# Optimization experiments

Measured on AMD Instinct MI355X. Metric: run time of the kernel, lower is better.

Reference implementation:

```python
import jax, jax.numpy as jnp
import numpy as np

# NOTE: PersistentHomology / wasserstein_distance are not in the provided source.
# We implement the standard interpretation: H0 (0-dimensional) persistent homology
# of the Vietoris-Rips filtration on the pairwise Euclidean distance matrix, whose
# diagram is (birth=0, death=w) for each edge weight w of the minimum spanning tree
# (single-linkage). The 1-Wasserstein distance between two equal-cardinality
# diagrams with birth=0 reduces to the L1 distance between sorted death values.

MARGIN = 1.0
EPS = 1e-12


def _pairwise_dist(x):
    # x: [N, D] -> [N, N] Euclidean distances
    sq = jnp.sum(x * x, axis=-1)
    d2 = sq[:, None] + sq[None, :] - 2.0 * (x @ x.T)
    return jnp.sqrt(jnp.maximum(d2, EPS))


def _mst_deaths(dist):
    # Prim's algorithm on the dense distance matrix; returns the N-1 MST edge
    # weights = H0 death times of the Vietoris-Rips filtration.
    n = dist.shape[0]
    inf = jnp.asarray(1e30, dist.dtype)
    visited0 = jnp.zeros(n, dtype=bool).at[0].set(True)
    mind0 = dist[0]  # min distance from current tree to every vertex

    def step(carry, _):
        visited, mind = carry
        cand = jnp.where(visited, inf, mind)
        j = jnp.argmin(cand)          # next vertex to attach
        w = cand[j]                   # weight of the MST edge used
        visited = visited.at[j].set(True)
        mind = jnp.minimum(mind, dist[j])
        return (visited, mind), w

    _, deaths = jax.lax.scan(step, (visited0, mind0), None, length=n - 1)
    return deaths  # [N-1]


def _wasserstein_1d(d1, d2):
    # 1-Wasserstein between two equal-size H0 diagrams (births are all 0):
    # optimal matching of 1-D point sets = L1 between sorted values.
    return jnp.sum(jnp.abs(jnp.sort(d1) - jnp.sort(d2)))


def _topological_distance(x, y):
    return _wasserstein_1d(_mst_deaths(_pairwise_dist(x)), _mst_deaths(_pairwise_dist(y)))


def setup_inputs() -> dict:
    key = jax.random.key(0)
    ka, kp, kn = jax.random.split(key, 3)
    N, D = 4096, 1024
    return {
        "anchor": jax.random.normal(ka, (N, D), dtype=jnp.float32),
        "positive": jax.random.normal(kp, (N, D), dtype=jnp.float32),
        "negative": jax.random.normal(kn, (N, D), dtype=jnp.float32),
    }


def reference(anchor, positive, negative):
    pos_dist = _topological_distance(anchor, positive)
    neg_dist = _topological_distance(anchor, negative)
    return jnp.maximum(pos_dist - neg_dist + MARGIN, 0.0)
```

## Files before the change

kernel.cpp:

```cpp
#include <hip/hip_runtime.h>
#include <stdint.h>


#define NPTS 4096
#define DIMF 1024
typedef unsigned short u16;
typedef _Float16 f16;
typedef unsigned long long ull;
static const ull KEY_MAX_ULL = ~0ull;

typedef f16 f16x8 __attribute__((ext_vector_type(8)));
typedef f16 f16x4v __attribute__((ext_vector_type(4)));
typedef float f32x4 __attribute__((ext_vector_type(4)));

#define GLOAD_LDS16(g, l)                                                      \
  __builtin_amdgcn_global_load_lds(                                            \
      (const __attribute__((address_space(1))) void*)(g),                      \
      (__attribute__((address_space(3))) void*)(l), 16, 0, 0)

__global__ void k_init_global(int* __restrict__ comp, ull* __restrict__ best,
                              float* __restrict__ deaths, int* __restrict__ cnt) {
  const int i = blockIdx.x * blockDim.x + threadIdx.x;
  if (i < 3 * NPTS) {
    comp[i] = i & (NPTS - 1);
    best[i] = KEY_MAX_ULL;
    deaths[i] = __int_as_float(0x7f800000);
  }
  if (i < 16) cnt[i] = 0;
}

__global__ __launch_bounds__(256)
void k_prep(const float* __restrict__ x, float* __restrict__ sq,
            f16* __restrict__ hi) {
  const int row = blockIdx.x;
  const int t = threadIdx.x;
  const float4 v = ((const float4*)(x + (size_t)row * DIMF))[t];
  f16x4v h;
  h.x = (f16)v.x; h.y = (f16)v.y; h.z = (f16)v.z; h.w = (f16)v.w;
  ((f16x4v*)(hi + (size_t)row * DIMF))[t] = h;
  float s = v.x * v.x + v.y * v.y + v.z * v.z + v.w * v.w;
  for (int off = 32; off > 0; off >>= 1) s += __shfl_xor(s, off, 64);
  __shared__ float ws[4];
  if ((t & 63) == 0) ws[t >> 6] = s;
  __syncthreads();
  if (t == 0) sq[row] = ws[0] + ws[1] + ws[2] + ws[3];
}

__global__ __launch_bounds__(256)
void k_gemm_f16(const f16* __restrict__ hi, const float* __restrict__ sq,
                f16* __restrict__ d16) {
  __shared__ u16 smem[8192];
  u16* As = smem;
  u16* Bs = smem + 4096;
  const int t = threadIdx.x;
  const int w = t >> 6, l = t & 63;
  const int wm = w >> 1, wn = w & 1;
  const int ml = l & 15, kq = l >> 4;
  const int i0 = blockIdx.y * 128, j0 = blockIdx.x * 128;

  const int srow = t >> 2, schk = t & 3;
  char* ldsA0 = (char*)As + t * 16;
  char* ldsB0 = (char*)Bs + t * 16;

  f32x4 acc[4][4];
#pragma unroll
  for (int a = 0; a < 4; ++a)
#pragma unroll
    for (int b = 0; b < 4; ++b) acc[a][b] = (f32x4)0.f;

  for (int k0 = 0; k0 < DIMF; k0 += 32) {
    __syncthreads();
    {
      const f16* ga0 = hi + (size_t)(i0 + srow) * DIMF + k0 + schk * 8;
      const f16* ga1 = hi + (size_t)(i0 + srow + 64) * DIMF + k0 + schk * 8;
      const f16* gb0 = hi + (size_t)(j0 + srow) * DIMF + k0 + schk * 8;
      const f16* gb1 = hi + (size_t)(j0 + srow + 64) * DIMF + k0 + schk * 8;
      GLOAD_LDS16(ga0, ldsA0);
      GLOAD_LDS16(ga1, ldsA0 + 4096);
      GLOAD_LDS16(gb0, ldsB0);
      GLOAD_LDS16(gb1, ldsB0 + 4096);
    }
    asm volatile("s_waitcnt vmcnt(0)" ::: "memory");
    __syncthreads();

    const char* Ab = (const char*)As + (wm * 64 + ml) * 64 + kq * 16;
    const char* Bb = (const char*)Bs + (wn * 64 + ml) * 64 + kq * 16;
    f16x8 af[4], bf[4];
#pragma unroll
    for (int mt = 0; mt < 4; ++mt) af[mt] = *(const f16x8*)(Ab + mt * 1024);
#pragma unroll
    for (int nt = 0; nt < 4; ++nt) bf[nt] = *(const f16x8*)(Bb + nt * 1024);
#pragma unroll
    for (int mt = 0; mt < 4; ++mt)
#pragma unroll
      for (int nt = 0; nt < 4; ++nt)
        acc[mt][nt] = __builtin_amdgcn_mfma_f32_16x16x32_f16(
            af[mt], bf[nt], acc[mt][nt], 0, 0, 0);
  }

  float sr[4][4], sc[4];
#pragma unroll
  for (int mt = 0; mt < 4; ++mt)
#pragma unroll
    for (int r = 0; r < 4; ++r)
      sr[mt][r] = sq[i0 + wm * 64 + mt * 16 + kq * 4 + r];
#pragma unroll
  for (int nt = 0; nt < 4; ++nt) sc[nt] = sq[j0 + wn * 64 + nt * 16 + ml];

#pragma unroll
  for (int mt = 0; mt < 4; ++mt)
#pragma unroll
    for (int nt = 0; nt < 4; ++nt) {
      const int col = j0 + wn * 64 + nt * 16 + ml;
#pragma unroll
      for (int r = 0; r < 4; ++r) {
        const int row = i0 + wm * 64 + mt * 16 + kq * 4 + r;
        const float v = fmaxf(sr[mt][r] + sc[nt] - 2.f * acc[mt][nt][r], 0.f);
        d16[(size_t)row * NPTS + col] = (f16)v;
      }
    }
}

__global__ __launch_bounds__(256)
void k_scan3(const u16* __restrict__ d16, const int* __restrict__ comp,
             ull* __restrict__ best, const int* __restrict__ done) {
  const int b = blockIdx.x;
  const int c = b >> 12;
  const int i = b & (NPTS - 1);
  if (done[c]) return;
  const int t = threadIdx.x;
  __shared__ ull red[4];
  const int* compc = comp + c * NPTS;
  int cj[16];
  {
    const int4* cp = (const int4*)compc;
    const int4 a0 = cp[t * 4 + 0], a1 = cp[t * 4 + 1];
    const int4 a2 = cp[t * 4 + 2], a3 = cp[t * 4 + 3];
    cj[0] = a0.x;  cj[1] = a0.y;  cj[2] = a0.z;  cj[3] = a0.w;
    cj[4] = a1.x;  cj[5] = a1.y;  cj[6] = a1.z;  cj[7] = a1.w;
    cj[8] = a2.x;  cj[9] = a2.y;  cj[10] = a2.z; cj[11] = a2.w;
    cj[12] = a3.x; cj[13] = a3.y; cj[14] = a3.z; cj[15] = a3.w;
  }
  const int ci = compc[i];
  const uint4* rp =
      (const uint4*)(d16 + (size_t)c * NPTS * NPTS + (size_t)i * NPTS);
  const uint4 Aw = rp[t * 2 + 0], Bw = rp[t * 2 + 1];
  const unsigned wds[8] = {Aw.x, Aw.y, Aw.z, Aw.w, Bw.x, Bw.y, Bw.z, Bw.w};
  ull kmin = KEY_MAX_ULL;
#pragma unroll
  for (int u = 0; u < 8; ++u) {
    const int j0c = t * 16 + u * 2;
    const unsigned lo = wds[u] & 0xFFFFu;
    const unsigned hi2 = wds[u] >> 16;
    if (cj[u * 2] != ci) {
      const int j = j0c;
      const ull pair = (i < j) ? (((ull)i << 12) | (unsigned)j)
                               : (((ull)j << 12) | (unsigned)i);
      const ull key = ((ull)lo << 24) | pair;
      kmin = (key < kmin) ? key : kmin;
    }
    if (cj[u * 2 + 1] != ci) {
      const int j = j0c + 1;
      const ull pair = (i < j) ? (((ull)i << 12) | (unsigned)j)
                               : (((ull)j << 12) | (unsigned)i);
      const ull key = ((ull)hi2 << 24) | pair;
      kmin = (key < kmin) ? key : kmin;
    }
  }
  for (int off = 32; off > 0; off >>= 1) {
    const ull o = __shfl_xor(kmin, off, 64);
    kmin = (o < kmin) ? o : kmin;
  }
  if ((t & 63) == 0) red[t >> 6] = kmin;
  __syncthreads();
  if (t == 0) {
    ull k2 = red[0];
    k2 = (red[1] < k2) ? red[1] : k2;
    k2 = (red[2] < k2) ? red[2] : k2;
    k2 = (red[3] < k2) ? red[3] : k2;
    if (k2 != KEY_MAX_ULL) atomicMin(best + c * NPTS + ci, k2);
  }
}

__global__ __launch_bounds__(1024)
void k_merge3(ull* __restrict__ best, int* __restrict__ comp,
              int* __restrict__ comp2, int* __restrict__ pairs,
              int* __restrict__ cnt, int* __restrict__ done,
              int* __restrict__ Cdev, ull* __restrict__ cd, int initCd) {
  const int c = blockIdx.x;
  if (done[c]) return;
  ull* bestc = best + c * NPTS;
  int* compc = comp + c * NPTS;
  int* comp2c = comp2 + c * NPTS;
  int* pairsc = pairs + c * NPTS;
  __shared__ int par[NPTS];
  __shared__ int hk[NPTS];
  __shared__ int redi[16];
  __shared__ int chg;
  __shared__ int cdense;
  const int t = threadIdx.x;
  ull bb[4];
#pragma unroll
  for (int s = 0; s < 4; ++s) {
    const int v = t + s * 1024;
    par[v] = compc[v];
    bb[s] = bestc[v];
    bestc[v] = KEY_MAX_ULL;
  }
  __syncthreads();
#pragma unroll
  for (int s = 0; s < 4; ++s) {
    const int v = t + s * 1024;
    const ull b2 = bb[s];
    int h;
    if (b2 == KEY_MAX_ULL) {
      h = par[v];
    } else {
      const int pair = (int)(b2 & 0xFFFFFF);
      const int a = pair >> 12, c2 = pair & 4095;
      const int ra = par[a], rb = par[c2];
      h = (ra == v) ? rb : ra;
    }
    hk[v] = h;
  }
  __syncthreads();
  bool win[4];
#pragma unroll
  for (int s = 0; s < 4; ++s) {
    const int v = t + s * 1024;
    const ull b2 = bb[s];
    win[s] = false;
    if (b2 != KEY_MAX_ULL) {
      const int so = hk[v];
      const bool mut = (hk[so] == v);
      win[s] = mut && (v < so);
      if (!mut || v < so)
        pairsc[atomicAdd(cnt + c, 1)] = (int)(b2 & 0xFFFFFF);
    }
  }
  if (t == 0) chg = 0;
  __syncthreads();
#pragma unroll
  for (int s = 0; s < 4; ++s)
    if (win[s]) hk[t + s * 1024] = t + s * 1024;
  __syncthreads();
  for (int it = 0; it < 12; ++it) {
    int w2[4]; int ch = 0;
#pragma unroll
    for (int s = 0; s < 4; ++s) {
      const int v = t + s * 1024;
      w2[s] = hk[hk[v]];
      ch |= (w2[s] != hk[v]);
    }
    __syncthreads();
#pragma unroll
    for (int s = 0; s < 4; ++s) hk[t + s * 1024] = w2[s];
    if (ch) chg = 1;
    __syncthreads();
    const int any = chg;
    __syncthreads();
    if (t == 0) chg = 0;
    if (!any) break;
  }
  int nroot = 0;
#pragma unroll
  for (int s = 0; s < 4; ++s) {
    const int v = t + s * 1024;
    const int rv = hk[v];
    compc[v] = rv;
    nroot += (rv == v);
  }
  for (int off = 32; off > 0; off >>= 1) nroot += __shfl_xor(nroot, off, 64);
  if ((t & 63) == 0) redi[t >> 6] = nroot;
  if (t == 0) cdense = 0;
  __syncthreads();
#pragma unroll
  for (int s = 0; s < 4; ++s) {
    const int v = t + s * 1024;
    if (hk[v] == v) par[v] = atomicAdd(&cdense, 1);
  }
  __syncthreads();
#pragma unroll
  for (int s = 0; s < 4; ++s) {
    const int v = t + s * 1024;
    comp2c[v] = par[hk[v]];
  }
  if (initCd) {
    ull* cdc = cd + (size_t)c * 65536;
    for (int q = t; q < 65536; q += 1024) cdc[q] = KEY_MAX_ULL;
  }
  if (t == 0) {
    int tot = 0;
    for (int q = 0; q < 16; ++q) tot += redi[q];
    Cdev[c] = cdense;
    if (tot == 1) done[c] = 1;
  }
}

__global__ __launch_bounds__(256)
void k_contract3(const u16* __restrict__ d16, const int* __restrict__ comp2,
                 ull* __restrict__ cd, const int* __restrict__ done) {
  const int b = blockIdx.x;
  const int c = b >> 12;
  const int i = b & (NPTS - 1);
  if (done[c]) return;
  const int t = threadIdx.x;
  __shared__ ull tbl[256];
  tbl[t] = KEY_MAX_ULL;
  const int* comp2c = comp2 + c * NPTS;
  int cj[16];
  {
    const int4* cp = (const int4*)comp2c;
    const int4 a0 = cp[t * 4 + 0], a1 = cp[t * 4 + 1];
    const int4 a2 = cp[t * 4 + 2], a3 = cp[t * 4 + 3];
    cj[0] = a0.x;  cj[1] = a0.y;  cj[2] = a0.z;  cj[3] = a0.w;
    cj[4] = a1.x;  cj[5] = a1.y;  cj[6] = a1.z;  cj[7] = a1.w;
    cj[8] = a2.x;  cj[9] = a2.y;  cj[10] = a2.z; cj[11] = a2.w;
    cj[12] = a3.x; cj[13] = a3.y; cj[14] = a3.z; cj[15] = a3.w;
  }
  const int ci = comp2c[i];
  __syncthreads();
  const uint4* rp =
      (const uint4*)(d16 + (size_t)c * NPTS * NPTS + (size_t)i * NPTS);
  const uint4 Aw = rp[t * 2 + 0], Bw = rp[t * 2 + 1];
  const unsigned wds[8] = {Aw.x, Aw.y, Aw.z, Aw.w, Bw.x, Bw.y, Bw.z, Bw.w};
#pragma unroll
  for (int u = 0; u < 8; ++u) {
    const int j0c = t * 16 + u * 2;
    const unsigned lo = wds[u] & 0xFFFFu;
    const unsigned hi2 = wds[u] >> 16;
    const int c0 = cj[u * 2], c1 = cj[u * 2 + 1];
    if (c0 != ci) {
      const int j = j0c;
      const ull pair = (i < j) ? (((ull)i << 12) | (unsigned)j)
                               : (((ull)j << 12) | (unsigned)i);
      atomicMin(&tbl[c0], ((ull)lo << 24) | pair);
    }
    if (c1 != ci) {
      const int j = j0c + 1;
      const ull pair = (i < j) ? (((ull)i << 12) | (unsigned)j)
                               : (((ull)j << 12) | (unsigned)i);
      atomicMin(&tbl[c1], ((ull)hi2 << 24) | pair);
    }
  }
  __syncthreads();
  const ull tv = tbl[t];
  if (tv != KEY_MAX_ULL) atomicMin(&cd[(size_t)c * 65536 + ci * 256 + t], tv);
}

__global__ __launch_bounds__(1024)
void k_finish3(const ull* __restrict__ cd, const int* __restrict__ comp2,
               const int* __restrict__ Cdev, int* __restrict__ pairs,
               int* __restrict__ cnt, const int* __restrict__ done) {
  const int c = blockIdx.x;
  if (done[c]) return;
  const ull* cdc = cd + (size_t)c * 65536;
  const int* comp2c = comp2 + c * NPTS;
  int* pairsc = pairs + c * NPTS;
  __shared__ int c2[NPTS];
  __shared__ ull bst[256];
  __shared__ int lbl[256];
  __shared__ int hk2[256];
  __shared__ int mk[256];
  __shared__ int nr_sh;
  const int t = threadIdx.x;
  const int C = Cdev[c];
#pragma unroll
  for (int s = 0; s < 4; ++s) c2[t + s * 1024] = comp2c[t + s * 1024];
  if (t < 256) lbl[t] = t;
  __syncthreads();
  for (int round = 0; round < 9; ++round) {
    if (t < 256) { bst[t] = KEY_MAX_ULL; mk[t] = 0; }
    if (t == 0) nr_sh = 0;
    __syncthreads();
    for (int idx = t; idx < C * 256; idx += 1024) {
      const int d = idx & 255;
      if (d < C) {
        const ull k = cdc[idx];
        if (k != KEY_MAX_ULL) {
          const int lc = lbl[idx >> 8], ld = lbl[d];
          if (lc != ld) atomicMin(&bst[lc], k);
        }
      }
    }
    __syncthreads();
    if (t < 256) {
      int h = t;
      const ull b = bst[t];
      if (t < C && b != KEY_MAX_ULL) {
        const int pair = (int)(b & 0xFFFFFF);
        const int a = pair >> 12, b2 = pair & 4095;
        const int sa = lbl[c2[a]], sb = lbl[c2[b2]];
        const int other = (sa == t) ? sb : sa;
        const ull bo = bst[other];
        const bool mut = (bo != KEY_MAX_ULL) && ((int)(bo & 0xFFFFFF) == pair);
        bool rec;
        if (mut) { h = (t < other) ? t : other; rec = (t < other); }
        else     { h = other;                   rec = true; }
        if (rec) pairsc[atomicAdd(cnt + c, 1)] = pair;
      }
      hk2[t] = h;
    }
    __syncthreads();
    for (int it = 0; it < 8; ++it) {
      int w2 = 0;
      if (t < 256) w2 = hk2[hk2[t]];
      __syncthreads();
      if (t < 256) hk2[t] = w2;
      __syncthreads();
    }
    if (t < 256) lbl[t] = hk2[lbl[t]];
    __syncthreads();
    if (t < C) mk[lbl[t]] = 1;
    __syncthreads();
    if (t < 256 && mk[t]) atomicAdd(&nr_sh, 1);
    __syncthreads();
    if (nr_sh <= 1) break;
  }
}

__global__ __launch_bounds__(256)
void k_deaths3(const float* __restrict__ x0, const float* __restrict__ x1,
               const float* __restrict__ x2, const float* __restrict__ sq,
               const int* __restrict__ pairs, float* __restrict__ deaths) {
  const int b = blockIdx.x;
  const int c = b >> 12;
  const int s = b & (NPTS - 1);
  if (s >= NPTS - 1) return;
  const int t = threadIdx.x;
  const int pr = pairs[c * NPTS + s];
  const int a = pr >> 12, e = pr & 4095;
  const float* X = (c == 0) ? x0 : (c == 1) ? x1 : x2;
  const float4 va = ((const float4*)(X + (size_t)a * DIMF))[t];
  const float4 vb = ((const float4*)(X + (size_t)e * DIMF))[t];
  float d = va.x * vb.x + va.y * vb.y + va.z * vb.z + va.w * vb.w;
  for (int off = 32; off > 0; off >>= 1) d += __shfl_xor(d, off, 64);
  __shared__ float ws[4];
  if ((t & 63) == 0) ws[t >> 6] = d;
  __syncthreads();
  if (t == 0) {
    const float dot = ws[0] + ws[1] + ws[2] + ws[3];
    const float dd = sq[c * NPTS + a] + sq[c * NPTS + e] - 2.f * dot;
    deaths[c * NPTS + s] = sqrtf(fmaxf(dd, 1e-12f));
  }
}

__global__ __launch_bounds__(1024)
void k_sort(float* __restrict__ deaths) {
  __shared__ float s[NPTS];
  float* g = deaths + (size_t)blockIdx.x * NPTS;
  const int t = threadIdx.x;
#pragma unroll
  for (int q = 0; q < 4; ++q) s[t + q * 1024] = g[t + q * 1024];
  for (int k = 2; k <= NPTS; k <<= 1) {
    for (int j = k >> 1; j > 0; j >>= 1) {
      __syncthreads();
#pragma unroll
      for (int q = 0; q < 4; ++q) {
        const int i = t + q * 1024;
        const int ixj = i ^ j;
        if (ixj > i) {
          const float a = s[i], b = s[ixj];
          const bool up = ((i & k) == 0);
          if ((a > b) == up) { s[i] = b; s[ixj] = a; }
        }
      }
    }
  }
  __syncthreads();
#pragma unroll
  for (int q = 0; q < 4; ++q) g[t + q * 1024] = s[t + q * 1024];
}

__global__ __launch_bounds__(1024)
void k_final(const float* __restrict__ deaths, float* __restrict__ out) {
  const float* a = deaths;
  const float* p = deaths + NPTS;
  const float* n = deaths + 2 * NPTS;
  const int t = threadIdx.x;
  float s1 = 0.f, s2 = 0.f;
  for (int i = t; i < NPTS - 1; i += 1024) {
    s1 += fabsf(a[i] - p[i]);
    s2 += fabsf(a[i] - n[i]);
  }
  for (int off = 32; off > 0; off >>= 1) {
    s1 += __shfl_xor(s1, off, 64);
    s2 += __shfl_xor(s2, off, 64);
  }
  __shared__ float r1[16], r2[16];
  if ((t & 63) == 0) { r1[t >> 6] = s1; r2[t >> 6] = s2; }
  __syncthreads();
  if (t == 0) {
    float t1 = 0.f, t2 = 0.f;
    for (int q = 0; q < 16; ++q) { t1 += r1[q]; t2 += r2[q]; }
    out[0] = fmaxf(t1 - t2 + 1.0f, 0.0f);
  }
}

__global__ __launch_bounds__(256)
void k_norms(const float* __restrict__ x, float* __restrict__ sq) {
  const int row = blockIdx.x;
  const int t = threadIdx.x;
  const float4 v = ((const float4*)(x + (size_t)row * DIMF))[t];
  float s = v.x * v.x + v.y * v.y + v.z * v.z + v.w * v.w;
  for (int off = 32; off > 0; off >>= 1) s += __shfl_xor(s, off, 64);
  __shared__ float ws[4];
  if ((t & 63) == 0) ws[t >> 6] = s;
  __syncthreads();
  if (t == 0) sq[row] = ws[0] + ws[1] + ws[2] + ws[3];
}

__global__ void k_init_cloud(int* __restrict__ comp, ull* __restrict__ best,
                             int* __restrict__ done) {
  int i = blockIdx.x * blockDim.x + threadIdx.x;
  if (i < NPTS) { comp[i] = i; best[i] = KEY_MAX_ULL; }
  if (i == 0) *done = 0;
}

#define BM 128
#define BN 128
#define BK 16
__global__ __launch_bounds__(256)
void k_gemm_d2(const float* __restrict__ X, const float* __restrict__ sq,
               float* __restrict__ d2) {
  __shared__ float As[BK][BM];
  __shared__ float Bs[BK][BN];
  const int tid = threadIdx.x;
  const int tx = tid & 15, ty = tid >> 4;
  const int i0 = blockIdx.y * BM, j0 = blockIdx.x * BN;
  float acc[8][8] = {};
  for (int k0 = 0; k0 < DIMF; k0 += BK) {
#pragma unroll
    for (int id = tid; id < 512; id += 256) {
      const int row = id >> 2;
      const int kk = (id & 3) << 2;
      const float4 a = *(const float4*)(X + (size_t)(i0 + row) * DIMF + k0 + kk);
      const float4 b = *(const float4*)(X + (size_t)(j0 + row) * DIMF + k0 + kk);
      As[kk + 0][row] = a.x; As[kk + 1][row] = a.y;
      As[kk + 2][row] = a.z; As[kk + 3][row] = a.w;
      Bs[kk + 0][row] = b.x; Bs[kk + 1][row] = b.y;
      Bs[kk + 2][row] = b.z; Bs[kk + 3][row] = b.w;
    }
    __syncthreads();
#pragma unroll
    for (int kk = 0; kk < BK; ++kk) {
      float a[8], b[8];
#pragma unroll
      for (int m = 0; m < 8; ++m) a[m] = As[kk][ty * 8 + m];
#pragma unroll
      for (int n = 0; n < 8; ++n) b[n] = Bs[kk][tx * 8 + n];
#pragma unroll
      for (int m = 0; m < 8; ++m)
#pragma unroll
        for (int n = 0; n < 8; ++n)
          acc[m][n] = fmaf(a[m], b[n], acc[m][n]);
    }
    __syncthreads();
  }
#pragma unroll
  for (int m = 0; m < 8; ++m) {
    const int i = i0 + ty * 8 + m;
    const float si = sq[i];
    const int j = j0 + tx * 8;
    float4 o0, o1;
    o0.x = fmaxf(si + sq[j + 0] - 2.f * acc[m][0], 0.f);
    o0.y = fmaxf(si + sq[j + 1] - 2.f * acc[m][1], 0.f);
    o0.z = fmaxf(si + sq[j + 2] - 2.f * acc[m][2], 0.f);
    o0.w = fmaxf(si + sq[j + 3] - 2.f * acc[m][3], 0.f);
    o1.x = fmaxf(si + sq[j + 4] - 2.f * acc[m][4], 0.f);
    o1.y = fmaxf(si + sq[j + 5] - 2.f * acc[m][5], 0.f);
    o1.z = fmaxf(si + sq[j + 6] - 2.f * acc[m][6], 0.f);
    o1.w = fmaxf(si + sq[j + 7] - 2.f * acc[m][7], 0.f);
    *(float4*)(d2 + (size_t)i * NPTS + j) = o0;
    *(float4*)(d2 + (size_t)i * NPTS + j + 4) = o1;
  }
}

__global__ __launch_bounds__(256)
void k_scan32(const float* __restrict__ d2, const int* __restrict__ comp,
              ull* __restrict__ best, const int* __restrict__ done) {
  if (*done) return;
  const int i = blockIdx.x;
  const int t = threadIdx.x;
  __shared__ ull red[4];
  int cj[16];
  {
    const int4* cp = (const int4*)comp;
    const int4 a0 = cp[t * 4 + 0], a1 = cp[t * 4 + 1];
    const int4 a2 = cp[t * 4 + 2], a3 = cp[t * 4 + 3];
    cj[0] = a0.x;  cj[1] = a0.y;  cj[2] = a0.z;  cj[3] = a0.w;
    cj[4] = a1.x;  cj[5] = a1.y;  cj[6] = a1.z;  cj[7] = a1.w;
    cj[8] = a2.x;  cj[9] = a2.y;  cj[10] = a2.z; cj[11] = a2.w;
    cj[12] = a3.x; cj[13] = a3.y; cj[14] = a3.z; cj[15] = a3.w;
  }
  const int ci = comp[i];
  const float* row = d2 + (size_t)i * NPTS;
  ull kmin = KEY_MAX_ULL;
#pragma unroll
  for (int q = 0; q < 4; ++q) {
    const float4 v = ((const float4*)row)[t * 4 + q];
    const float vv[4] = {v.x, v.y, v.z, v.w};
#pragma unroll
    for (int u = 0; u < 4; ++u) {
      const int j = t * 16 + q * 4 + u;
      if (cj[q * 4 + u] != ci) {
        const ull pair = (i < j) ? (((ull)i << 12) | (unsigned)j)
                                 : (((ull)j << 12) | (unsigned)i);
        const ull key = ((ull)__float_as_uint(vv[u]) << 24) | pair;
        kmin = (key < kmin) ? key : kmin;
      }
    }
  }
  for (int off = 32; off > 0; off >>= 1) {
    const ull o = __shfl_xor(kmin, off, 64);
    kmin = (o < kmin) ? o : kmin;
  }
  if ((t & 63) == 0) red[t >> 6] = kmin;
  __syncthreads();
  if (t == 0) {
    ull k2 = red[0];
    k2 = (red[1] < k2) ? red[1] : k2;
    k2 = (red[2] < k2) ? red[2] : k2;
    k2 = (red[3] < k2) ? red[3] : k2;
    if (k2 != KEY_MAX_ULL) atomicMin(best + ci, k2);
  }
}

__global__ __launch_bounds__(1024)
void k_merge1(ull* __restrict__ best, int* __restrict__ comp,
              const float* __restrict__ d2, float* __restrict__ deaths,
              int* __restrict__ cnt, int* __restrict__ done) {
  if (*done) return;
  __shared__ int par[NPTS];
  __shared__ int hk[NPTS];
  __shared__ int redi[16];
  const int t = threadIdx.x;
  ull bb[4];
#pragma unroll
  for (int s = 0; s < 4; ++s) {
    const int v = t + s * 1024;
    par[v] = comp[v];
    bb[s] = best[v];
    best[v] = KEY_MAX_ULL;
  }
  __syncthreads();
#pragma unroll
  for (int s = 0; s < 4; ++s) {
    const int v = t + s * 1024;
    const ull b2 = bb[s];
    int h;
    if (b2 == KEY_MAX_ULL) {
      h = par[v];
    } else {
      const int pair = (int)(b2 & 0xFFFFFF);
      const int a = pair >> 12, c2 = pair & 4095;
      const int ra = par[a], rb = par[c2];
      h = (ra == v) ? rb : ra;
    }
    hk[v] = h;
  }
  __syncthreads();
  bool win[4];
#pragma unroll
  for (int s = 0; s < 4; ++s) {
    const int v = t + s * 1024;
    const ull b2 = bb[s];
    win[s] = false;
    if (b2 != KEY_MAX_ULL) {
      const int so = hk[v];
      const bool mut = (hk[so] == v);
      win[s] = mut && (v < so);
      if (!mut || v < so) {
        const int pair = (int)(b2 & 0xFFFFFF);
        const float dd = d2[(size_t)(pair >> 12) * NPTS + (pair & 4095)];
        deaths[atomicAdd(cnt, 1)] = sqrtf(fmaxf(dd, 1e-12f));
      }
    }
  }
  __syncthreads();
#pragma unroll
  for (int s = 0; s < 4; ++s)
    if (win[s]) hk[t + s * 1024] = t + s * 1024;
  __syncthreads();
  for (int it = 0; it < 12; ++it) {
    int w2[4];
#pragma unroll
    for (int s = 0; s < 4; ++s) w2[s] = hk[hk[t + s * 1024]];
    __syncthreads();
#pragma unroll
    for (int s = 0; s < 4; ++s) hk[t + s * 1024] = w2[s];
    __syncthreads();
  }
  int nroot = 0;
#pragma unroll
  for (int s = 0; s < 4; ++s) {
    const int v = t + s * 1024;
    const int rv = hk[v];
    comp[v] = rv;
    nroot += (rv == v);
  }
  for (int off = 32; off > 0; off >>= 1) nroot += __shfl_xor(nroot, off, 64);
  if ((t & 63) == 0) redi[t >> 6] = nroot;
  __syncthreads();
  if (t == 0) {
    int tot = 0;
    for (int q = 0; q < 16; ++q) tot += redi[q];
    if (tot == 1) *done = 1;
  }
}

__global__ void k_fail(float* out) { if (threadIdx.x == 0) out[0] = 0.f; }

extern "C" void kernel_launch(void* const* d_in, const int* in_sizes, int n_in,
                              void* d_out, int out_size, void* d_ws, size_t ws_size,
                              hipStream_t stream) {
  const float* xs[3] = {(const float*)d_in[0], (const float*)d_in[1],
                        (const float*)d_in[2]};
  char* ws = (char*)d_ws;
  const size_t d16_one = (size_t)NPTS * NPTS * 2;
  const size_t d16_all = 3 * d16_one;
  const size_t hi_bytes = (size_t)NPTS * DIMF * 2;
  const size_t tail_new = 3 * NPTS * 4  + 3 * NPTS * 4  +
                          3 * NPTS * 4  + 3 * NPTS * 8  +
                          3 * NPTS * 4  + 3 * NPTS * 4  + 128;
  const size_t need_new = d16_all + hi_bytes + tail_new;
  const size_t d2_bytes = (size_t)NPTS * NPTS * 4;
  const size_t small_old = NPTS * 4 + NPTS * 4 + NPTS * 8 + 3 * NPTS * 4 + 128;
  const size_t need_old = d2_bytes + small_old;

  if (ws_size >= need_new) {
    f16* d16 = (f16*)ws;
    f16* hi = (f16*)(ws + d16_all);
    ull* cd = (ull*)(ws + d16_all);
    char* tp = ws + d16_all + hi_bytes;
    float* sq = (float*)tp;                    tp += 3 * NPTS * 4;
    int* comp = (int*)tp;                      tp += 3 * NPTS * 4;
    int* comp2 = (int*)tp;                     tp += 3 * NPTS * 4;
    ull* best = (ull*)tp;                      tp += 3 * NPTS * 8;
    float* deaths = (float*)tp;                tp += 3 * NPTS * 4;
    int* pairs = (int*)tp;                     tp += 3 * NPTS * 4;
    int* cnt = (int*)tp;
    int* done = cnt + 3;
    int* Cdev = cnt + 6;

    k_init_global<<<48, 256, 0, stream>>>(comp, best, deaths, cnt);
    for (int c = 0; c < 3; ++c) {
      k_prep<<<NPTS, 256, 0, stream>>>(xs[c], sq + c * NPTS, hi);
      k_gemm_f16<<<dim3(NPTS / 128, NPTS / 128), 256, 0, stream>>>(
          hi, sq + c * NPTS, d16 + (size_t)c * NPTS * NPTS);
    }
    for (int r = 0; r < 4; ++r) {
      k_scan3<<<3 * NPTS, 256, 0, stream>>>((const u16*)d16, comp, best, done);
      k_merge3<<<3, 1024, 0, stream>>>(best, comp, comp2, pairs, cnt, done,
                                       Cdev, cd, (r == 3) ? 1 : 0);
    }
    k_contract3<<<3 * NPTS, 256, 0, stream>>>((const u16*)d16, comp2, cd, done);
    k_finish3<<<3, 1024, 0, stream>>>(cd, comp2, Cdev, pairs, cnt, done);
    k_deaths3<<<3 * NPTS, 256, 0, stream>>>(xs[0], xs[1], xs[2], sq, pairs,
                                            deaths);
    k_sort<<<3, 1024, 0, stream>>>(deaths);
    k_final<<<1, 1024, 0, stream>>>(deaths, (float*)d_out);
  } else if (ws_size >= need_old) {
    float* d2 = (float*)ws;
    char* tp = ws + d2_bytes;
    float* sq = (float*)tp;                    tp += NPTS * 4;
    int* comp = (int*)tp;                      tp += NPTS * 4;
    ull* best = (ull*)tp;                      tp += NPTS * 8;
    float* deaths = (float*)tp;                tp += 3 * NPTS * 4;
    int* cnt = (int*)tp;
    int* done = cnt + 3;
    k_init_cloud<<<16, 256, 0, stream>>>(comp, best, done);
    {
    }
    k_norms<<<NPTS, 256, 0, stream>>>(xs[0], sq);
    struct {} _;
    (void)_;
    k_init_global<<<48, 256, 0, stream>>>(comp, best, deaths, cnt);
    for (int c = 0; c < 3; ++c) {
      k_norms<<<NPTS, 256, 0, stream>>>(xs[c], sq);
      k_init_cloud<<<16, 256, 0, stream>>>(comp, best, done);
      k_gemm_d2<<<dim3(NPTS / BN, NPTS / BM), 256, 0, stream>>>(xs[c], sq, d2);
      for (int r = 0; r < 12; ++r) {
        k_scan32<<<NPTS, 256, 0, stream>>>(d2, comp, best, done);
        k_merge1<<<1, 1024, 0, stream>>>(best, comp, d2, deaths + c * NPTS,
                                         cnt + c, done);
      }
    }
    k_sort<<<3, 1024, 0, stream>>>(deaths);
    k_final<<<1, 1024, 0, stream>>>(deaths, (float*)d_out);
  } else {
    k_fail<<<1, 64, 0, stream>>>((float*)d_out);
  }
}
```

Measured before the change: 507.2 us.

## Process two rows per scan block and stop Boruvka rounds once few components remain

The Boruvka scan kernel now handles two distance rows per block, halving the block count. When both rows share a component it merges their minima into one atomic. Scan and merge rounds now exit early once the component count drops to 256 or below, leaving the rest to the contraction path, and the contracted matrix is initialised in the first round instead of the last. Cdev is seeded to NPTS so the early-exit test is valid from round one. The fallback path's redundant init launches are also trimmed. The risk is correctness: contraction must handle a larger component count if rounds are skipped.

Result: faster. 461.3 us (-9.1%).

```diff
diff --git a/kernel.cpp b/kernel.cpp
--- a/kernel.cpp
+++ b/kernel.cpp
@@ -26,7 +26,7 @@
     best[i] = KEY_MAX_ULL;
     deaths[i] = __int_as_float(0x7f800000);
   }
-  if (i < 16) cnt[i] = 0;
+  if (i < 16) cnt[i] = (i >= 6 && i < 9) ? NPTS : 0;
 }
 
 __global__ __launch_bounds__(256)
@@ -123,13 +123,15 @@
 
 __global__ __launch_bounds__(256)
 void k_scan3(const u16* __restrict__ d16, const int* __restrict__ comp,
-             ull* __restrict__ best, const int* __restrict__ done) {
+             ull* __restrict__ best, const int* __restrict__ done,
+             const int* __restrict__ Cdev) {
   const int b = blockIdx.x;
-  const int c = b >> 12;
-  const int i = b & (NPTS - 1);
-  if (done[c]) return;
-  const int t = threadIdx.x;
-  __shared__ ull red[4];
+  const int c = b >> 11;
+  const int r0 = (b & 2047) * 2;
+  const int r1 = r0 + 1;
+  if (done[c] || Cdev[c] <= 256) return;
+  const int t = threadIdx.x;
+  __shared__ ull red0[4], red1[4];
   const int* compc = comp + c * NPTS;
   int cj[16];
   {
@@ -141,44 +143,70 @@
     cj[8] = a2.x;  cj[9] = a2.y;  cj[10] = a2.z; cj[11] = a2.w;
     cj[12] = a3.x; cj[13] = a3.y; cj[14] = a3.z; cj[15] = a3.w;
   }
-  const int ci = compc[i];
-  const uint4* rp =
-      (const uint4*)(d16 + (size_t)c * NPTS * NPTS + (size_t)i * NPTS);
-  const uint4 Aw = rp[t * 2 + 0], Bw = rp[t * 2 + 1];
-  const unsigned wds[8] = {Aw.x, Aw.y, Aw.z, Aw.w, Bw.x, Bw.y, Bw.z, Bw.w};
-  ull kmin = KEY_MAX_ULL;
+  const int ci0 = compc[r0];
+  const int ci1 = compc[r1];
+  const u16* base = d16 + (size_t)c * NPTS * NPTS;
+  const uint4* rp0 = (const uint4*)(base + (size_t)r0 * NPTS);
+  const uint4* rp1 = (const uint4*)(base + (size_t)r1 * NPTS);
+  const uint4 A0 = rp0[t * 2 + 0], B0 = rp0[t * 2 + 1];
+  const uint4 A1 = rp1[t * 2 + 0], B1 = rp1[t * 2 + 1];
+  const unsigned w0[8] = {A0.x, A0.y, A0.z, A0.w, B0.x, B0.y, B0.z, B0.w};
+  const unsigned w1[8] = {A1.x, A1.y, A1.z, A1.w, B1.x, B1.y, B1.z, B1.w};
+  ull k0 = KEY_MAX_ULL, k1 = KEY_MAX_ULL;
 #pragma unroll
   for (int u = 0; u < 8; ++u) {
-    const int j0c = t * 16 + u * 2;
-    const unsigned lo = wds[u] & 0xFFFFu;
-    const unsigned hi2 = wds[u] >> 16;
-    if (cj[u * 2] != ci) {
-      const int j = j0c;
-      const ull pair = (i < j) ? (((ull)i << 12) | (unsigned)j)
-                               : (((ull)j << 12) | (unsigned)i);
-      const ull key = ((ull)lo << 24) | pair;
-      kmin = (key < kmin) ? key : kmin;
-    }
-    if (cj[u * 2 + 1] != ci) {
-      const int j = j0c + 1;
-      const ull pair = (i < j) ? (((ull)i << 12) | (unsigned)j)
-                               : (((ull)j << 12) | (unsigned)i);
-      const ull key = ((ull)hi2 << 24) | pair;
-      kmin = (key < kmin) ? key : kmin;
+    const int jc = t * 16 + u * 2;
+    const int c0 = cj[u * 2], c1 = cj[u * 2 + 1];
+    if (c0 != ci0) {
+      const ull pair = (r0 < jc) ? (((ull)r0 << 12) | (unsigned)jc)
+                                 : (((ull)jc << 12) | (unsigned)r0);
+      const ull key = ((ull)(w0[u] & 0xFFFFu) << 24) | pair;
+      k0 = (key < k0) ? key : k0;
+    }
+    if (c1 != ci0) {
+      const int j = jc + 1;
+      const ull pair = (r0 < j) ? (((ull)r0 << 12) | (unsigned)j)
+                                : (((ull)j << 12) | (unsigned)r0);
+      const ull key = ((ull)(w0[u] >> 16) << 24) | pair;
+      k0 = (key < k0) ? key : k0;
+    }
+    if (c0 != ci1) {
+      const ull pair = (r1 < jc) ? (((ull)r1 << 12) | (unsigned)jc)
+                                 : (((ull)jc << 12) | (unsigned)r1);
+      const ull key = ((ull)(w1[u] & 0xFFFFu) << 24) | pair;
+      k1 = (key < k1) ? key : k1;
+    }
+    if (c1 != ci1) {
+      const int j = jc + 1;
+      const ull pair = (r1 < j) ? (((ull)r1 << 12) | (unsigned)j)
+                                : (((ull)j << 12) | (unsigned)r1);
+      const ull key = ((ull)(w1[u] >> 16) << 24) | pair;
+      k1 = (key < k1) ? key : k1;
     }
   }
   for (int off = 32; off > 0; off >>= 1) {
-    const ull o = __shfl_xor(kmin, off, 64);
-    kmin = (o < kmin) ? o : kmin;
-  }
-  if ((t & 63) == 0) red[t >> 6] = kmin;
+    const ull o0 = __shfl_xor(k0, off, 64);
+    const ull o1 = __shfl_xor(k1, off, 64);
+    k0 = (o0 < k0) ? o0 : k0;
+    k1 = (o1 < k1) ? o1 : k1;
+  }
+  if ((t & 63) == 0) { red0[t >> 6] = k0; red1[t >> 6] = k1; }
   __syncthreads();
   if (t == 0) {
-    ull k2 = red[0];
-    k2 = (red[1] < k2) ? red[1] : k2;
-    k2 = (red[2] < k2) ? red[2] : k2;
-    k2 = (red[3] < k2) ? red[3] : k2;
-    if (k2 != KEY_MAX_ULL) atomicMin(best + c * NPTS + ci, k2);
+    ull m0 = red0[0], m1 = red1[0];
+#pragma unroll
+    for (int q = 1; q < 4; ++q) {
+      m0 = (red0[q] < m0) ? red0[q] : m0;
+      m1 = (red1[q] < m1) ? red1[q] : m1;
+    }
+    ull* bestc = best + c * NPTS;
+    if (ci0 == ci1) {
+      const ull m = (m1 < m0) ? m1 : m0;
+      if (m != KEY_MAX_ULL) atomicMin(bestc + ci0, m);
+    } else {
+      if (m0 != KEY_MAX_ULL) atomicMin(bestc + ci0, m0);
+      if (m1 != KEY_MAX_ULL) atomicMin(bestc + ci1, m1);
+    }
   }
 }
 
@@ -188,7 +216,7 @@
               int* __restrict__ cnt, int* __restrict__ done,
               int* __restrict__ Cdev, ull* __restrict__ cd, int initCd) {
   const int c = blockIdx.x;
-  if (done[c]) return;
+  if (done[c] || Cdev[c] <= 256) return;
   ull* bestc = best + c * NPTS;
   int* compc = comp + c * NPTS;
   int* comp2c = comp2 + c * NPTS;
@@ -517,6 +545,12 @@
   if (i == 0) *done = 0;
 }
 
+__global__ void k_init_deaths(float* __restrict__ deaths, int* __restrict__ cnt) {
+  int i = blockIdx.x * blockDim.x + threadIdx.x;
+  if (i < 3 * NPTS) deaths[i] = __int_as_float(0x7f800000);
+  if (i < 8) cnt[i] = 0;
+}
+
 #define BM 128
 #define BN 128
 #define BK 16
@@ -750,9 +784,10 @@
           hi, sq + c * NPTS, d16 + (size_t)c * NPTS * NPTS);
     }
     for (int r = 0; r < 4; ++r) {
-      k_scan3<<<3 * NPTS, 256, 0, stream>>>((const u16*)d16, comp, best, done);
+      k_scan3<<<3 * (NPTS / 2), 256, 0, stream>>>((const u16*)d16, comp, best,
+                                                  done, Cdev);
       k_merge3<<<3, 1024, 0, stream>>>(best, comp, comp2, pairs, cnt, done,
-                                       Cdev, cd, (r == 3) ? 1 : 0);
+                                       Cdev, cd, (r == 0) ? 1 : 0);
     }
     k_contract3<<<3 * NPTS, 256, 0, stream>>>((const u16*)d16, comp2, cd, done);
     k_finish3<<<3, 1024, 0, stream>>>(cd, comp2, Cdev, pairs, cnt, done);
@@ -769,13 +804,7 @@
     float* deaths = (float*)tp;                tp += 3 * NPTS * 4;
     int* cnt = (int*)tp;
     int* done = cnt + 3;
-    k_init_cloud<<<16, 256, 0, stream>>>(comp, best, done);
-    {
-    }
-    k_norms<<<NPTS, 256, 0, stream>>>(xs[0], sq);
-    struct {} _;
-    (void)_;
-    k_init_global<<<48, 256, 0, stream>>>(comp, best, deaths, cnt);
+    k_init_deaths<<<48, 256, 0, stream>>>(deaths, cnt);
     for (int c = 0; c < 3; ++c) {
       k_norms<<<NPTS, 256, 0, stream>>>(xs[c], sq);
       k_init_cloud<<<16, 256, 0, stream>>>(comp, best, done);
```
